# Kernel optimization log

Hardware: AMD Instinct MI355X
Metric: run time of the kernel (lower is better)

## Reference

```python
import jax, jax.numpy as jnp
import numpy as np

B, C, HC, H, W = 4, 512, 64, 64, 64


def _spectral_norm(Wm, u):
    # one torch-style power iteration; u,v are treated as constants (detached)
    v = Wm.T @ u
    v = v / jnp.maximum(jnp.linalg.norm(v), 1e-12)
    u2 = Wm @ v
    u2 = u2 / jnp.maximum(jnp.linalg.norm(u2), 1e-12)
    u2 = jax.lax.stop_gradient(u2)
    v = jax.lax.stop_gradient(v)
    sigma = u2 @ (Wm @ v)
    return Wm / sigma


def setup_inputs() -> dict:
    key = jax.random.key(0)
    ks = jax.random.split(key, 14)
    return {
        "x": jax.random.normal(ks[0], (B, C, H, W), jnp.float32),
        "Wf": jax.random.normal(ks[1], (HC, C), jnp.float32) * 0.05,
        "bf": jax.random.normal(ks[2], (HC,), jnp.float32) * 0.05,
        "Wg": jax.random.normal(ks[3], (HC, C), jnp.float32) * 0.05,
        "bg": jax.random.normal(ks[4], (HC,), jnp.float32) * 0.05,
        "Wh": jax.random.normal(ks[5], (HC, C), jnp.float32) * 0.05,
        "bh": jax.random.normal(ks[6], (HC,), jnp.float32) * 0.05,
        "Wv": jax.random.normal(ks[7], (C, HC), jnp.float32) * 0.05,
        "bv": jax.random.normal(ks[8], (C,), jnp.float32) * 0.05,
        "uf": jax.random.normal(ks[9], (HC,), jnp.float32),
        "ug": jax.random.normal(ks[10], (HC,), jnp.float32),
        "uh": jax.random.normal(ks[11], (HC,), jnp.float32),
        "uv": jax.random.normal(ks[12], (C,), jnp.float32),
        "gamma": jax.random.normal(ks[13], (1,), jnp.float32),
    }


def reference(x, Wf, bf, Wg, bg, Wh, bh, Wv, bv, uf, ug, uh, uv, gamma):
    nb, nc, imgh, imgw = x.shape
    n = imgh * imgw
    xf = x.reshape(nb, nc, n)  # [B, C, N]
    Wf_sn = _spectral_norm(Wf, uf)
    Wg_sn = _spectral_norm(Wg, ug)
    Wh_sn = _spectral_norm(Wh, uh)
    Wv_sn = _spectral_norm(Wv, uv)
    # 1x1 convs are per-pixel GEMMs
    f = jnp.einsum('kc,bcn->bkn', Wf_sn, xf) + bf[:, None]  # [B, HC, N]
    g = jnp.einsum('kc,bcn->bkn', Wg_sn, xf) + bg[:, None]
    h = jnp.einsum('kc,bcn->bkn', Wh_sn, xf) + bh[:, None]
    s = jnp.einsum('bkn,bkm->bnm', f, g)       # [B, N, N] scores
    beta = jax.nn.softmax(s, axis=-1)
    o = jnp.einsum('bnm,bkm->bkn', beta, h)    # [B, HC, N] (already transposed)
    out = jnp.einsum('ck,bkn->bcn', Wv_sn, o) + bv[:, None]
    out = out.reshape(nb, nc, imgh, imgw)
    return gamma[0] * out + x
```

## Files before the change

kernel.cpp:

```cpp
#include <hip/hip_runtime.h>
#include <hip/hip_bf16.h>

typedef __attribute__((ext_vector_type(8))) short short8;
typedef __attribute__((ext_vector_type(4))) float floatx4;
typedef __attribute__((ext_vector_type(16))) float floatx16;
typedef unsigned short ushortt;

#define LOG2E 1.4426950408889634f

__device__ __forceinline__ float fast_exp2(float x) {
    return __builtin_amdgcn_exp2f(x);
}
__device__ __forceinline__ ushortt f2bf(float f) {
    unsigned int u = __float_as_uint(f);
    u += 0x7fffu + ((u >> 16) & 1u);
    return (ushortt)(u >> 16);
}
__device__ __forceinline__ unsigned int f2bf_pk(float a, float b) {
    float2 t; t.x = a; t.y = b;
    __hip_bfloat162 h = __float22bfloat162_rn(t);
    return *reinterpret_cast<unsigned int*>(&h);
}
__device__ __forceinline__ float bf2f(ushortt h) {
    return __uint_as_float(((unsigned int)h) << 16);
}

__device__ __forceinline__ float block_sum(float v, float* red) {
    #pragma unroll
    for (int off = 32; off > 0; off >>= 1) v += __shfl_down(v, off);
    int wid = threadIdx.x >> 6, ln = threadIdx.x & 63;
    __syncthreads();
    if (ln == 0) red[wid] = v;
    __syncthreads();
    return red[0] + red[1] + red[2] + red[3];
}

__global__ __launch_bounds__(256) void sigma_kernel(
    const float* __restrict__ Wf, const float* __restrict__ uf,
    const float* __restrict__ Wg, const float* __restrict__ ug,
    const float* __restrict__ Wh, const float* __restrict__ uh,
    const float* __restrict__ Wv, const float* __restrict__ uv,
    float* __restrict__ sig) {
    __shared__ float tv[512];
    __shared__ float tvp[256];
    __shared__ float zpart[256];
    __shared__ float red[4];
    const int mat = blockIdx.x, tid = threadIdx.x;

    if (mat < 3) {
        const float* W = (mat == 0) ? Wf : ((mat == 1) ? Wg : Wh);
        const float* u = (mat == 0) ? uf : ((mat == 1) ? ug : uh);
        for (int c = tid; c < 512; c += 256) {
            float s0 = 0.f;
            #pragma unroll 8
            for (int r = 0; r < 64; ++r) s0 += W[r * 512 + c] * u[r];
            tv[c] = s0;
        }
        __syncthreads();
        float p = tv[tid] * tv[tid] + tv[tid + 256] * tv[tid + 256];
        float nt2 = block_sum(p, red);
        float nt = fmaxf(sqrtf(nt2), 1e-12f);
        {
            int r = tid & 63, qq = tid >> 6;
            const float* Wr = W + r * 512 + qq * 128;
            const float* tq = tv + qq * 128;
            float part = 0.f;
            #pragma unroll 16
            for (int c = 0; c < 128; ++c) part += Wr[c] * tq[c];
            zpart[tid] = part;
        }
        __syncthreads();
        if (tid < 64) {
            float z = zpart[tid] + zpart[tid + 64] + zpart[tid + 128] + zpart[tid + 192];
            z = z * z;
            #pragma unroll
            for (int off = 32; off > 0; off >>= 1) z += __shfl_xor(z, off);
            if (tid == 0) sig[mat] = sqrtf(z) / nt;
        }
    } else {
        const float* W = Wv; const float* u = uv;
        {
            int c = tid & 63, rs = tid >> 6;
            float s0 = 0.f;
            #pragma unroll 8
            for (int r = rs * 128; r < rs * 128 + 128; ++r) s0 += W[r * 64 + c] * u[r];
            tvp[tid] = s0;
        }
        __syncthreads();
        if (tid < 64) tv[tid] = tvp[tid] + tvp[tid + 64] + tvp[tid + 128] + tvp[tid + 192];
        __syncthreads();
        float t = (tid < 64) ? tv[tid] : 0.f;
        float nt2 = block_sum(t * t, red);
        float nt = fmaxf(sqrtf(nt2), 1e-12f);
        {
            const float* w1 = W + (size_t)tid * 64;
            const float* w2 = W + (size_t)(tid + 256) * 64;
            float z1 = 0.f, z2 = 0.f;
            #pragma unroll 8
            for (int c = 0; c < 64; ++c) {
                float tc = tv[c];
                z1 += w1[c] * tc;
                z2 += w2[c] * tc;
            }
            float zp = z1 * z1 + z2 * z2;
            float z2t = block_sum(zp, red);
            if (tid == 0) sig[3] = sqrtf(z2t) / nt;
        }
    }
}

__global__ __launch_bounds__(256) void prep_w_kernel(
    const float* __restrict__ Wf, const float* __restrict__ Wg,
    const float* __restrict__ Wh, const float* __restrict__ Wv,
    const float* __restrict__ sig,
    ushortt* __restrict__ wqkv, ushortt* __restrict__ wvb) {
    int idx = blockIdx.x * 256 + threadIdx.x;
    if (idx < 98304) {
        int k = idx >> 9, c = idx & 511;
        int which = k >> 6;
        const float* W = (which == 0) ? Wf : ((which == 1) ? Wg : Wh);
        float inv = 1.0f / sig[which];
        wqkv[idx] = f2bf(W[(k & 63) * 512 + c] * inv);
    } else {
        int o = idx - 98304;
        wvb[o] = f2bf(Wv[o] / sig[3]);
    }
}

__global__ __launch_bounds__(256, 4) void qkv_kernel(
    const float* __restrict__ x, const ushortt* __restrict__ wqkv,
    const float* __restrict__ bfv, const float* __restrict__ bgv,
    const float* __restrict__ bhv,
    ushortt* __restrict__ Qb, ushortt* __restrict__ Kb, ushortt* __restrict__ Vt) {
    __shared__ unsigned int xs[1120];
    const int tid = threadIdx.x;
    const int n0 = blockIdx.x * 32, b = blockIdx.y;
    const int lane = tid & 63, w = tid >> 6;
    const int strip = w & 1, ksel = w >> 1;
    const int q = lane >> 4, l15 = lane & 15;
    const int sn = tid & 31, sg = tid >> 5;

    floatx4 acc[6];
    #pragma unroll
    for (int kt = 0; kt < 6; ++kt) acc[kt] = (floatx4){0.f, 0.f, 0.f, 0.f};

    const float* xb = x + ((size_t)b * 512) * 4096 + n0 + sn;
    float2 pre[4];
    #pragma unroll
    for (int i = 0; i < 4; ++i) {
        int c = sg * 8 + 2 * i;
        pre[i].x = xb[(size_t)c * 4096];
        pre[i].y = xb[(size_t)(c + 1) * 4096];
    }

    for (int c0 = 0; c0 < 512; c0 += 64) {
        __syncthreads();
        {
            uint4 pk;
            pk.x = f2bf_pk(pre[0].x, pre[0].y);
            pk.y = f2bf_pk(pre[1].x, pre[1].y);
            pk.z = f2bf_pk(pre[2].x, pre[2].y);
            pk.w = f2bf_pk(pre[3].x, pre[3].y);
            *reinterpret_cast<uint4*>(&xs[sn * 32 + ((sg ^ (sn & 7)) << 2)]) = pk;
        }
        if (c0 + 64 < 512) {
            #pragma unroll
            for (int i = 0; i < 4; ++i) {
                int c = c0 + 64 + sg * 8 + 2 * i;
                pre[i].x = xb[(size_t)c * 4096];
                pre[i].y = xb[(size_t)(c + 1) * 4096];
            }
        }
        __syncthreads();
        const unsigned int* xr = &xs[(16 * strip + l15) * 32];
        #pragma unroll
        for (int kc = 0; kc < 2; ++kc) {
            union { uint4 v; short8 s8; } af;
            af.v = *reinterpret_cast<const uint4*>(&xr[((4 * kc + q) ^ (l15 & 7)) << 2]);
            #pragma unroll
            for (int kt = 0; kt < 6; ++kt) {
                short8 bb = *reinterpret_cast<const short8*>(
                    &wqkv[(size_t)(ksel * 96 + kt * 16 + l15) * 512 + c0 + kc * 32 + q * 8]);
                acc[kt] = __builtin_amdgcn_mfma_f32_16x16x32_bf16(af.s8, bb, acc[kt], 0, 0, 0);
            }
        }
    }

    const int nloc = n0 + 16 * strip + 4 * q;
    if (ksel == 0) {
        #pragma unroll
        for (int kt = 0; kt < 4; ++kt) {
            int k = kt * 16 + l15;
            float bb = bfv[k];
            #pragma unroll
            for (int r = 0; r < 4; ++r)
                Qb[((size_t)b * 4096 + nloc + r) * 64 + k] = f2bf((acc[kt][r] + bb) * LOG2E);
        }
        #pragma unroll
        for (int kt = 4; kt < 6; ++kt) {
            int k = (kt - 4) * 16 + l15;
            float bb = bgv[k];
            #pragma unroll
            for (int r = 0; r < 4; ++r)
                Kb[((size_t)b * 4096 + nloc + r) * 64 + k] = f2bf(acc[kt][r] + bb);
        }
    } else {
        #pragma unroll
        for (int kt = 0; kt < 2; ++kt) {
            int k = 32 + kt * 16 + l15;
            float bb = bgv[k];
            #pragma unroll
            for (int r = 0; r < 4; ++r)
                Kb[((size_t)b * 4096 + nloc + r) * 64 + k] = f2bf(acc[kt][r] + bb);
        }
    }
    __syncthreads();
    if (ksel == 1) {
        #pragma unroll
        for (int kt = 2; kt < 6; ++kt) {
            int d = (kt - 2) * 16 + l15;
            float bb = bhv[d];
            int base = d * 17 + 8 * strip + 2 * q;
            xs[base]     = f2bf_pk(acc[kt][0] + bb, acc[kt][1] + bb);
            xs[base + 1] = f2bf_pk(acc[kt][2] + bb, acc[kt][3] + bb);
        }
    }
    __syncthreads();
    {
        int d = tid >> 2, sgg = tid & 3;
        uint4 vv;
        vv.x = xs[d * 17 + sgg * 4 + 0]; vv.y = xs[d * 17 + sgg * 4 + 1];
        vv.z = xs[d * 17 + sgg * 4 + 2]; vv.w = xs[d * 17 + sgg * 4 + 3];
        *reinterpret_cast<uint4*>(&Vt[((size_t)b * 64 + d) * 4096 + n0 + sgg * 8]) = vv;
    }
}

__global__ __launch_bounds__(256, 3) void attn_kernel(
    const ushortt* __restrict__ Qb, const ushortt* __restrict__ Kb,
    const ushortt* __restrict__ Vt, ushortt* __restrict__ Opart,
    float2* __restrict__ ml, ushortt* __restrict__ Ob, int KB) {
    __shared__ unsigned int smem[4420];
    const int tid = threadIdx.x;
    const int n0 = blockIdx.x * 64, b = blockIdx.y, s = blockIdx.z;
    const int lane = tid & 63, w = tid >> 6;
    const int qh = w & 1, kh = w >> 1;
    const int l31 = lane & 31, h = lane >> 5;

    const ushortt* Kg = Kb + (size_t)b * 4096 * 64;
    const ushortt* Vg = Vt + (size_t)b * 64 * 4096;

    short8 bq[4];
    {
        const ushortt* Qg = Qb + ((size_t)b * 4096 + n0 + 32 * qh + l31) * 64;
        #pragma unroll
        for (int kc = 0; kc < 4; ++kc)
            bq[kc] = *reinterpret_cast<const short8*>(Qg + kc * 16 + 8 * h);
    }

    floatx16 ot0 = {}, ot1 = {};
    float m_i = -1e30f, l_i = 0.f;

    const int row = tid >> 2, seg = tid & 3;
    const int kbeg = s * KB, kend = kbeg + KB;

    uint4 ck0, ck1, cv0, cv1;
    {
        int nb = kbeg * 64;
        const ushortt* kp = Kg + (size_t)(nb + row) * 64 + seg * 16;
        ck0 = *reinterpret_cast<const uint4*>(kp);
        ck1 = *reinterpret_cast<const uint4*>(kp + 8);
        const ushortt* vp = Vg + (size_t)row * 4096 + nb + seg * 16;
        cv0 = *reinterpret_cast<const uint4*>(vp);
        cv1 = *reinterpret_cast<const uint4*>(vp + 8);
    }

    const int rsw = row & 7;
    for (int kb = kbeg; kb < kend; ++kb) {
        __syncthreads();
        {
            *reinterpret_cast<uint4*>(&smem[row * 32 + (((2 * seg) ^ rsw) << 2)]) = ck0;
            *reinterpret_cast<uint4*>(&smem[row * 32 + (((2 * seg + 1) ^ rsw) << 2)]) = ck1;
            *reinterpret_cast<uint4*>(&smem[2048 + row * 32 + (((2 * seg) ^ rsw) << 2)]) = cv0;
            *reinterpret_cast<uint4*>(&smem[2048 + row * 32 + (((2 * seg + 1) ^ rsw) << 2)]) = cv1;
        }
        if (kb + 1 < kend) {
            int nb = (kb + 1) * 64;
            const ushortt* kp = Kg + (size_t)(nb + row) * 64 + seg * 16;
            ck0 = *reinterpret_cast<const uint4*>(kp);
            ck1 = *reinterpret_cast<const uint4*>(kp + 8);
            const ushortt* vp = Vg + (size_t)row * 4096 + nb + seg * 16;
            cv0 = *reinterpret_cast<const uint4*>(vp);
            cv1 = *reinterpret_cast<const uint4*>(vp + 8);
        }
        __syncthreads();

        floatx16 st = {};
        const unsigned int* kr = &smem[(32 * kh + l31) * 32];
        const int esw = l31 & 7;
        #pragma unroll
        for (int kc = 0; kc < 4; ++kc) {
            union { uint4 v; short8 s8; } af;
            af.v = *reinterpret_cast<const uint4*>(&kr[((2 * kc + h) ^ esw) << 2]);
            st = __builtin_amdgcn_mfma_f32_32x32x16_bf16(af.s8, bq[kc], st, 0, 0, 0);
        }

        float mx = st[0];
        #pragma unroll
        for (int r = 1; r < 16; ++r) mx = fmaxf(mx, st[r]);
        mx = fmaxf(mx, __shfl_xor(mx, 32));
        if (__any(mx > m_i)) {
            float mn = fmaxf(m_i, mx);
            float alpha = fast_exp2(m_i - mn);
            m_i = mn;
            l_i *= alpha;
            #pragma unroll
            for (int r = 0; r < 16; ++r) { ot0[r] *= alpha; ot1[r] *= alpha; }
        }
        float p[16], rs = 0.f;
        #pragma unroll
        for (int r = 0; r < 16; ++r) { p[r] = fast_exp2(st[r] - m_i); rs += p[r]; }
        rs += __shfl_xor(rs, 32);
        l_i += rs;

        unsigned int pk[8], sp[8];
        #pragma unroll
        for (int i = 0; i < 8; ++i) pk[i] = f2bf_pk(p[2 * i], p[2 * i + 1]);
        #pragma unroll
        for (int i = 0; i < 8; ++i) sp[i] = (unsigned int)__shfl_xor((int)pk[i], 32);
        union { unsigned int u[4]; short8 s8; } pb0, pb1;
        pb0.u[0] = h ? sp[2] : pk[0]; pb0.u[1] = h ? sp[3] : pk[1];
        pb0.u[2] = h ? pk[2] : sp[0]; pb0.u[3] = h ? pk[3] : sp[1];
        pb1.u[0] = h ? sp[6] : pk[4]; pb1.u[1] = h ? sp[7] : pk[5];
        pb1.u[2] = h ? pk[6] : sp[4]; pb1.u[3] = h ? pk[7] : sp[5];

        const unsigned int* vr0 = &smem[2048 + l31 * 32];
        const unsigned int* vr1 = &smem[2048 + (32 + l31) * 32];
        #pragma unroll
        for (int c = 0; c < 2; ++c) {
            union { uint4 v; short8 s8; } af;
            af.v = *reinterpret_cast<const uint4*>(&vr0[((4 * kh + 2 * c + h) ^ esw) << 2]);
            ot0 = __builtin_amdgcn_mfma_f32_32x32x16_bf16(af.s8, c ? pb1.s8 : pb0.s8, ot0, 0, 0, 0);
            af.v = *reinterpret_cast<const uint4*>(&vr1[((4 * kh + 2 * c + h) ^ esw) << 2]);
            ot1 = __builtin_amdgcn_mfma_f32_32x32x16_bf16(af.s8, c ? pb1.s8 : pb0.s8, ot1, 0, 0, 0);
        }
    }

    __syncthreads();
    if (h == 0) {
        smem[4160 + w * 32 + l31] = __float_as_uint(m_i);
        smem[4288 + w * 32 + l31] = __float_as_uint(l_i);
    }
    __syncthreads();
    int pw = 2 * (1 - kh) + qh;
    float m2 = __uint_as_float(smem[4160 + pw * 32 + l31]);
    float l2 = __uint_as_float(smem[4288 + pw * 32 + l31]);
    float mstar = fmaxf(m_i, m2);
    float wself = fast_exp2(m_i - mstar);
    float w2 = fast_exp2(m2 - mstar);
    float lm = wself * l_i + w2 * l2;
    float sc = (gridDim.z == 1) ? (wself / lm) : wself;
    if (gridDim.z > 1 && kh == 0 && h == 0) {
        float2 v; v.x = mstar; v.y = lm;
        ml[((size_t)s * 4 + b) * 4096 + n0 + 32 * qh + l31] = v;
    }
    float* om = reinterpret_cast<float*>(smem);
    if (kh == 0) {
        #pragma unroll
        for (int r = 0; r < 16; ++r) {
            int d0 = (r & 3) + 8 * (r >> 2) + 4 * h;
            om[(32 * qh + l31) * 65 + d0] = sc * ot0[r];
            om[(32 * qh + l31) * 65 + 32 + d0] = sc * ot1[r];
        }
    }
    __syncthreads();
    if (kh == 1) {
        #pragma unroll
        for (int r = 0; r < 16; ++r) {
            int d0 = (r & 3) + 8 * (r >> 2) + 4 * h;
            om[(32 * qh + l31) * 65 + d0] += sc * ot0[r];
            om[(32 * qh + l31) * 65 + 32 + d0] += sc * ot1[r];
        }
    }
    __syncthreads();
    {
        int qq = tid >> 2, dsg = tid & 3;
        unsigned int pkk[8];
        #pragma unroll
        for (int j = 0; j < 8; ++j)
            pkk[j] = f2bf_pk(om[qq * 65 + dsg * 16 + 2 * j], om[qq * 65 + dsg * 16 + 2 * j + 1]);
        ushortt* base = (gridDim.z == 1)
            ? (Ob + ((size_t)b * 4096 + n0) * 64)
            : (Opart + (((size_t)s * 4 + b) * 4096 + n0) * 64);
        uint4* d4 = reinterpret_cast<uint4*>(base + (size_t)qq * 64 + dsg * 16);
        uint4 o0; o0.x = pkk[0]; o0.y = pkk[1]; o0.z = pkk[2]; o0.w = pkk[3];
        uint4 o1; o1.x = pkk[4]; o1.y = pkk[5]; o1.z = pkk[6]; o1.w = pkk[7];
        d4[0] = o0; d4[1] = o1;
    }
}

__global__ __launch_bounds__(256) void combine_kernel(
    const ushortt* __restrict__ Opart, const float2* __restrict__ ml,
    ushortt* __restrict__ Ob, int S) {
    const int tid = threadIdx.x;
    const int n0 = blockIdx.x * 64, b = blockIdx.y;
    const int row = n0 + (tid >> 2), dseg = tid & 3;
    float2 mls[4];
    float m = -1e30f;
    for (int s = 0; s < S; ++s) {
        mls[s] = ml[((size_t)s * 4 + b) * 4096 + row];
        m = fmaxf(m, mls[s].x);
    }
    float wgt[4], denom = 0.f;
    for (int s = 0; s < S; ++s) {
        wgt[s] = fast_exp2(mls[s].x - m);
        denom += wgt[s] * mls[s].y;
    }
    float inv = 1.0f / denom;
    float acc[16];
    #pragma unroll
    for (int j = 0; j < 16; ++j) acc[j] = 0.f;
    for (int s = 0; s < S; ++s) {
        const uint4* op = reinterpret_cast<const uint4*>(
            Opart + (((size_t)s * 4 + b) * 4096 + row) * 64 + dseg * 16);
        union { uint4 v; ushortt hh[8]; } u0, u1;
        u0.v = op[0]; u1.v = op[1];
        float ww = wgt[s];
        #pragma unroll
        for (int j = 0; j < 8; ++j) {
            acc[j] += ww * bf2f(u0.hh[j]);
            acc[8 + j] += ww * bf2f(u1.hh[j]);
        }
    }
    union { uint4 u[2]; unsigned int ww[8]; } pkv;
    #pragma unroll
    for (int j = 0; j < 8; ++j) pkv.ww[j] = f2bf_pk(acc[2 * j] * inv, acc[2 * j + 1] * inv);
    uint4* dst = reinterpret_cast<uint4*>(Ob + ((size_t)b * 4096 + row) * 64 + dseg * 16);
    dst[0] = pkv.u[0]; dst[1] = pkv.u[1];
}

__global__ __launch_bounds__(256) void proj_kernel(
    const ushortt* __restrict__ Ob, const ushortt* __restrict__ wvb,
    const float* __restrict__ bv, const float* __restrict__ gamma,
    const float* __restrict__ x, float* __restrict__ out) {
    const int tid = threadIdx.x;
    const int n0 = blockIdx.y * 64, c0 = blockIdx.x * 64, b = blockIdx.z;
    const int w = tid >> 6, lane = tid & 63, q = lane >> 4, l15 = lane & 15;

    short8 a0 = *reinterpret_cast<const short8*>(&wvb[(size_t)(c0 + 16 * w + l15) * 64 + q * 8]);
    short8 a1 = *reinterpret_cast<const short8*>(&wvb[(size_t)(c0 + 16 * w + l15) * 64 + 32 + q * 8]);
    floatx4 acc[4];
    #pragma unroll
    for (int t = 0; t < 4; ++t) acc[t] = (floatx4){0.f, 0.f, 0.f, 0.f};
    #pragma unroll
    for (int t = 0; t < 4; ++t) {
        const ushortt* ob = Ob + ((size_t)b * 4096 + n0 + 16 * t + l15) * 64;
        short8 b0 = *reinterpret_cast<const short8*>(ob + q * 8);
        short8 b1 = *reinterpret_cast<const short8*>(ob + 32 + q * 8);
        acc[t] = __builtin_amdgcn_mfma_f32_16x16x32_bf16(a0, b0, acc[t], 0, 0, 0);
        acc[t] = __builtin_amdgcn_mfma_f32_16x16x32_bf16(a1, b1, acc[t], 0, 0, 0);
    }
    float gm = gamma[0];
    #pragma unroll
    for (int t = 0; t < 4; ++t) {
        #pragma unroll
        for (int r = 0; r < 4; ++r) {
            int c = c0 + 16 * w + 4 * q + r;
            int n = n0 + 16 * t + l15;
            size_t idx = ((size_t)(b * 512 + c)) * 4096 + n;
            out[idx] = gm * (acc[t][r] + bv[c]) + x[idx];
        }
    }
}

extern "C" void kernel_launch(void* const* d_in, const int* in_sizes, int n_in,
                              void* d_out, int out_size, void* d_ws, size_t ws_size,
                              hipStream_t stream) {
    const float* x   = (const float*)d_in[0];
    const float* Wf  = (const float*)d_in[1];
    const float* bf_ = (const float*)d_in[2];
    const float* Wg  = (const float*)d_in[3];
    const float* bg_ = (const float*)d_in[4];
    const float* Wh  = (const float*)d_in[5];
    const float* bh_ = (const float*)d_in[6];
    const float* Wv  = (const float*)d_in[7];
    const float* bv_ = (const float*)d_in[8];
    const float* uf  = (const float*)d_in[9];
    const float* ug  = (const float*)d_in[10];
    const float* uh  = (const float*)d_in[11];
    const float* uv  = (const float*)d_in[12];
    const float* gm  = (const float*)d_in[13];
    float* out = (float*)d_out;

    char* ws = (char*)d_ws;
    float*   sig   = (float*)ws;
    ushortt* wqkv  = (ushortt*)(ws + 256);
    ushortt* wvb   = (ushortt*)(ws + 196864);
    ushortt* Qb    = (ushortt*)(ws + 262400);
    ushortt* Kb    = (ushortt*)(ws + 2359552);
    ushortt* Vt    = (ushortt*)(ws + 4456704);
    ushortt* Ob    = (ushortt*)(ws + 6553856);
    float2*  ml    = (float2*)(ws + 8651008);
    ushortt* Opart = (ushortt*)(ws + 9175296);

    int S = (ws_size >= (size_t)17563904) ? 4 : 1;

    sigma_kernel<<<4, 256, 0, stream>>>(Wf, uf, Wg, ug, Wh, uh, Wv, uv, sig);
    prep_w_kernel<<<512, 256, 0, stream>>>(Wf, Wg, Wh, Wv, sig, wqkv, wvb);
    qkv_kernel<<<dim3(128, 4), 256, 0, stream>>>(x, wqkv, bf_, bg_, bh_, Qb, Kb, Vt);
    attn_kernel<<<dim3(64, 4, S), 256, 0, stream>>>(Qb, Kb, Vt, Opart, ml, Ob, 64 / S);
    if (S > 1) combine_kernel<<<dim3(64, 4), 256, 0, stream>>>(Opart, ml, Ob, S);
    proj_kernel<<<dim3(8, 64, 4), 256, 0, stream>>>(Ob, wvb, bv_, gm, x, out);
}
```

Before: 219.1 us.

## Double-buffer LDS in qkv and attn kernels, vectorize proj epilogue

```diff
diff --git a/kernel.cpp b/kernel.cpp
--- a/kernel.cpp
+++ b/kernel.cpp
@@ -132,7 +132,7 @@
     const float* __restrict__ bfv, const float* __restrict__ bgv,
     const float* __restrict__ bhv,
     ushortt* __restrict__ Qb, ushortt* __restrict__ Kb, ushortt* __restrict__ Vt) {
-    __shared__ unsigned int xs[1120];
+    __shared__ unsigned int xs[2048];
     const int tid = threadIdx.x;
     const int n0 = blockIdx.x * 32, b = blockIdx.y;
     const int lane = tid & 63, w = tid >> 6;
@@ -145,6 +145,7 @@
     for (int kt = 0; kt < 6; ++kt) acc[kt] = (floatx4){0.f, 0.f, 0.f, 0.f};
 
     const float* xb = x + ((size_t)b * 512) * 4096 + n0 + sn;
+    const int sslot = sn * 32 + ((sg ^ (sn & 7)) << 2);
     float2 pre[4];
     #pragma unroll
     for (int i = 0; i < 4; ++i) {
@@ -152,27 +153,41 @@
         pre[i].x = xb[(size_t)c * 4096];
         pre[i].y = xb[(size_t)(c + 1) * 4096];
     }
-
-    for (int c0 = 0; c0 < 512; c0 += 64) {
+    {
+        uint4 pk;
+        pk.x = f2bf_pk(pre[0].x, pre[0].y);
+        pk.y = f2bf_pk(pre[1].x, pre[1].y);
+        pk.z = f2bf_pk(pre[2].x, pre[2].y);
+        pk.w = f2bf_pk(pre[3].x, pre[3].y);
+        *reinterpret_cast<uint4*>(&xs[sslot]) = pk;
+    }
+    #pragma unroll
+    for (int i = 0; i < 4; ++i) {
+        int c = 64 + sg * 8 + 2 * i;
+        pre[i].x = xb[(size_t)c * 4096];
+        pre[i].y = xb[(size_t)(c + 1) * 4096];
+    }
+
+    for (int it = 0; it < 8; ++it) {
         __syncthreads();
-        {
+        if (it < 7) {
             uint4 pk;
             pk.x = f2bf_pk(pre[0].x, pre[0].y);
             pk.y = f2bf_pk(pre[1].x, pre[1].y);
             pk.z = f2bf_pk(pre[2].x, pre[2].y);
             pk.w = f2bf_pk(pre[3].x, pre[3].y);
-            *reinterpret_cast<uint4*>(&xs[sn * 32 + ((sg ^ (sn & 7)) << 2)]) = pk;
-        }
-        if (c0 + 64 < 512) {
+            *reinterpret_cast<uint4*>(&xs[(((it + 1) & 1) << 10) + sslot]) = pk;
+        }
+        if (it < 6) {
             #pragma unroll
             for (int i = 0; i < 4; ++i) {
-                int c = c0 + 64 + sg * 8 + 2 * i;
+                int c = (it + 2) * 64 + sg * 8 + 2 * i;
                 pre[i].x = xb[(size_t)c * 4096];
                 pre[i].y = xb[(size_t)(c + 1) * 4096];
             }
         }
-        __syncthreads();
-        const unsigned int* xr = &xs[(16 * strip + l15) * 32];
+        const int c0 = it * 64;
+        const unsigned int* xr = &xs[((it & 1) << 10) + (16 * strip + l15) * 32];
         #pragma unroll
         for (int kc = 0; kc < 2; ++kc) {
             union { uint4 v; short8 s8; } af;
@@ -239,7 +254,7 @@
     const ushortt* __restrict__ Qb, const ushortt* __restrict__ Kb,
     const ushortt* __restrict__ Vt, ushortt* __restrict__ Opart,
     float2* __restrict__ ml, ushortt* __restrict__ Ob, int KB) {
-    __shared__ unsigned int smem[4420];
+    __shared__ unsigned int smem[8448];
     const int tid = threadIdx.x;
     const int n0 = blockIdx.x * 64, b = blockIdx.y, s = blockIdx.z;
     const int lane = tid & 63, w = tid >> 6;
@@ -262,6 +277,9 @@
 
     const int row = tid >> 2, seg = tid & 3;
     const int kbeg = s * KB, kend = kbeg + KB;
+    const int rsw = row & 7;
+    const int ws0 = row * 32 + ((((2 * seg)) ^ rsw) << 2);
+    const int ws1 = row * 32 + ((((2 * seg + 1)) ^ rsw) << 2);
 
     uint4 ck0, ck1, cv0, cv1;
     {
@@ -273,18 +291,33 @@
         cv0 = *reinterpret_cast<const uint4*>(vp);
         cv1 = *reinterpret_cast<const uint4*>(vp + 8);
     }
-
-    const int rsw = row & 7;
+    *reinterpret_cast<uint4*>(&smem[ws0]) = ck0;
+    *reinterpret_cast<uint4*>(&smem[ws1]) = ck1;
+    *reinterpret_cast<uint4*>(&smem[2048 + ws0]) = cv0;
+    *reinterpret_cast<uint4*>(&smem[2048 + ws1]) = cv1;
+    if (kbeg + 1 < kend) {
+        int nb = (kbeg + 1) * 64;
+        const ushortt* kp = Kg + (size_t)(nb + row) * 64 + seg * 16;
+        ck0 = *reinterpret_cast<const uint4*>(kp);
+        ck1 = *reinterpret_cast<const uint4*>(kp + 8);
+        const ushortt* vp = Vg + (size_t)row * 4096 + nb + seg * 16;
+        cv0 = *reinterpret_cast<const uint4*>(vp);
+        cv1 = *reinterpret_cast<const uint4*>(vp + 8);
+    }
+
     for (int kb = kbeg; kb < kend; ++kb) {
+        const int cur = (kb - kbeg) & 1;
+        const unsigned int rb = cur ? 4096u : 0u;
+        const unsigned int wbs = cur ? 0u : 4096u;
         __syncthreads();
-        {
-            *reinterpret_cast<uint4*>(&smem[row * 32 + (((2 * seg) ^ rsw) << 2)]) = ck0;
-            *reinterpret_cast<uint4*>(&smem[row * 32 + (((2 * seg + 1) ^ rsw) << 2)]) = ck1;
-            *reinterpret_cast<uint4*>(&smem[2048 + row * 32 + (((2 * seg) ^ rsw) << 2)]) = cv0;
-            *reinterpret_cast<uint4*>(&smem[2048 + row * 32 + (((2 * seg + 1) ^ rsw) << 2)]) = cv1;
-        }
         if (kb + 1 < kend) {
-            int nb = (kb + 1) * 64;
+            *reinterpret_cast<uint4*>(&smem[wbs + ws0]) = ck0;
+            *reinterpret_cast<uint4*>(&smem[wbs + ws1]) = ck1;
+            *reinterpret_cast<uint4*>(&smem[wbs + 2048 + ws0]) = cv0;
+            *reinterpret_cast<uint4*>(&smem[wbs + 2048 + ws1]) = cv1;
+        }
+        if (kb + 2 < kend) {
+            int nb = (kb + 2) * 64;
             const ushortt* kp = Kg + (size_t)(nb + row) * 64 + seg * 16;
             ck0 = *reinterpret_cast<const uint4*>(kp);
             ck1 = *reinterpret_cast<const uint4*>(kp + 8);
@@ -292,10 +325,9 @@
             cv0 = *reinterpret_cast<const uint4*>(vp);
             cv1 = *reinterpret_cast<const uint4*>(vp + 8);
         }
-        __syncthreads();
 
         floatx16 st = {};
-        const unsigned int* kr = &smem[(32 * kh + l31) * 32];
+        const unsigned int* kr = &smem[rb + (32 * kh + l31) * 32];
         const int esw = l31 & 7;
         #pragma unroll
         for (int kc = 0; kc < 4; ++kc) {
@@ -304,11 +336,13 @@
             st = __builtin_amdgcn_mfma_f32_32x32x16_bf16(af.s8, bq[kc], st, 0, 0, 0);
         }
 
-        float mx = st[0];
-        #pragma unroll
-        for (int r = 1; r < 16; ++r) mx = fmaxf(mx, st[r]);
+        float mx = fmaxf(fmaxf(fmaxf(st[0], st[1]), fmaxf(st[2], st[3])),
+                         fmaxf(fmaxf(st[4], st[5]), fmaxf(st[6], st[7])));
+        float mx2 = fmaxf(fmaxf(fmaxf(st[8], st[9]), fmaxf(st[10], st[11])),
+                          fmaxf(fmaxf(st[12], st[13]), fmaxf(st[14], st[15])));
+        mx = fmaxf(mx, mx2);
         mx = fmaxf(mx, __shfl_xor(mx, 32));
-        if (__any(mx > m_i)) {
+        if (!__all(mx <= m_i + 8.f)) {
             float mn = fmaxf(m_i, mx);
             float alpha = fast_exp2(m_i - mn);
             m_i = mn;
@@ -333,8 +367,8 @@
         pb1.u[0] = h ? sp[6] : pk[4]; pb1.u[1] = h ? sp[7] : pk[5];
         pb1.u[2] = h ? pk[6] : sp[4]; pb1.u[3] = h ? pk[7] : sp[5];
 
-        const unsigned int* vr0 = &smem[2048 + l31 * 32];
-        const unsigned int* vr1 = &smem[2048 + (32 + l31) * 32];
+        const unsigned int* vr0 = &smem[rb + 2048 + l31 * 32];
+        const unsigned int* vr1 = &smem[rb + 2048 + (32 + l31) * 32];
         #pragma unroll
         for (int c = 0; c < 2; ++c) {
             union { uint4 v; short8 s8; } af;
@@ -347,13 +381,13 @@
 
     __syncthreads();
     if (h == 0) {
-        smem[4160 + w * 32 + l31] = __float_as_uint(m_i);
-        smem[4288 + w * 32 + l31] = __float_as_uint(l_i);
+        smem[8192 + w * 32 + l31] = __float_as_uint(m_i);
+        smem[8320 + w * 32 + l31] = __float_as_uint(l_i);
     }
     __syncthreads();
     int pw = 2 * (1 - kh) + qh;
-    float m2 = __uint_as_float(smem[4160 + pw * 32 + l31]);
-    float l2 = __uint_as_float(smem[4288 + pw * 32 + l31]);
+    float m2 = __uint_as_float(smem[8192 + pw * 32 + l31]);
+    float l2 = __uint_as_float(smem[8320 + pw * 32 + l31]);
     float mstar = fmaxf(m_i, m2);
     float wself = fast_exp2(m_i - mstar);
     float w2 = fast_exp2(m2 - mstar);
@@ -442,6 +476,7 @@
     const ushortt* __restrict__ Ob, const ushortt* __restrict__ wvb,
     const float* __restrict__ bv, const float* __restrict__ gamma,
     const float* __restrict__ x, float* __restrict__ out) {
+    __shared__ float ps[64 * 65];
     const int tid = threadIdx.x;
     const int n0 = blockIdx.y * 64, c0 = blockIdx.x * 64, b = blockIdx.z;
     const int w = tid >> 6, lane = tid & 63, q = lane >> 4, l15 = lane & 15;
@@ -459,16 +494,29 @@
         acc[t] = __builtin_amdgcn_mfma_f32_16x16x32_bf16(a0, b0, acc[t], 0, 0, 0);
         acc[t] = __builtin_amdgcn_mfma_f32_16x16x32_bf16(a1, b1, acc[t], 0, 0, 0);
     }
+    #pragma unroll
+    for (int t = 0; t < 4; ++t) {
+        #pragma unroll
+        for (int r = 0; r < 4; ++r)
+            ps[(16 * w + 4 * q + r) * 65 + 16 * t + l15] = acc[t][r];
+    }
+    __syncthreads();
     float gm = gamma[0];
-    #pragma unroll
-    for (int t = 0; t < 4; ++t) {
-        #pragma unroll
-        for (int r = 0; r < 4; ++r) {
-            int c = c0 + 16 * w + 4 * q + r;
-            int n = n0 + 16 * t + l15;
-            size_t idx = ((size_t)(b * 512 + c)) * 4096 + n;
-            out[idx] = gm * (acc[t][r] + bv[c]) + x[idx];
-        }
+    const int cl = tid >> 4;
+    const int n4 = (tid & 15) * 4;
+    #pragma unroll
+    for (int p = 0; p < 4; ++p) {
+        int c = c0 + p * 16 + cl;
+        float bb = bv[c];
+        size_t idx = ((size_t)(b * 512 + c)) * 4096 + n0 + n4;
+        float4 xv = *reinterpret_cast<const float4*>(&x[idx]);
+        const float* pr = &ps[(p * 16 + cl) * 65 + n4];
+        float4 ov;
+        ov.x = gm * (pr[0] + bb) + xv.x;
+        ov.y = gm * (pr[1] + bb) + xv.y;
+        ov.z = gm * (pr[2] + bb) + xv.z;
+        ov.w = gm * (pr[3] + bb) + xv.w;
+        *reinterpret_cast<float4*>(&out[idx]) = ov;
     }
 }
 
```

Result: no change. 216.6 us (-1.1%).
